# Kernel optimization log

Measured on AMD Instinct MI355X. Metric: run time of the kernel, lower is better.

The kernel has to match this reference:

```python
import jax, jax.numpy as jnp
import numpy as np

B, N, K, D, F, H = 8, 512, 16, 256, 1024, 8


def _ln(x, g, b):
    m = jnp.mean(x, axis=-1, keepdims=True)
    v = jnp.var(x, axis=-1, keepdims=True)
    return (x - m) / jnp.sqrt(v + 1e-5) * g + b


def _mlp(x, W1, b1, W2, b2):
    return jax.nn.gelu(x @ W1 + b1, approximate=False) @ W2 + b2


def setup_inputs() -> dict:
    key = jax.random.key(0)
    ks = jax.random.split(key, 16)
    s = 0.02
    inp = {
        'x': jax.random.normal(ks[0], (N, B, D), jnp.float32),
        'e': jax.random.normal(ks[1], (B, N, K, D), jnp.float32),
        'edge_index': jax.random.randint(ks[2], (B, N, K), 0, N),
        'Wq': jax.random.normal(ks[3], (D, D), jnp.float32) * s,
        'bq': jnp.zeros((D,), jnp.float32),
        'Wk': jax.random.normal(ks[4], (D, D), jnp.float32) * s,
        'bk': jnp.zeros((D,), jnp.float32),
        'Wv': jax.random.normal(ks[5], (D, D), jnp.float32) * s,
        'bv': jnp.zeros((D,), jnp.float32),
        'Wo': jax.random.normal(ks[6], (D, D), jnp.float32) * s,
        'bo': jnp.zeros((D,), jnp.float32),
        'nW1': jax.random.normal(ks[7], (D, F), jnp.float32) * s,
        'nb1': jnp.zeros((F,), jnp.float32),
        'nW2': jax.random.normal(ks[8], (F, D), jnp.float32) * s,
        'nb2': jnp.zeros((D,), jnp.float32),
        'eW1': jax.random.normal(ks[9], (D, F), jnp.float32) * s,
        'eb1': jnp.zeros((F,), jnp.float32),
        'eW2': jax.random.normal(ks[10], (F, D), jnp.float32) * s,
        'eb2': jnp.zeros((D,), jnp.float32),
        'na_g': jnp.ones((D,), jnp.float32), 'na_b': jnp.zeros((D,), jnp.float32),
        'ea_g': jnp.ones((D,), jnp.float32), 'ea_b': jnp.zeros((D,), jnp.float32),
        'nf_g': jnp.ones((D,), jnp.float32), 'nf_b': jnp.zeros((D,), jnp.float32),
        'ef_g': jnp.ones((D,), jnp.float32), 'ef_b': jnp.zeros((D,), jnp.float32),
    }
    return inp


def reference(x, e, edge_index, Wq, bq, Wk, bk, Wv, bv, Wo, bo,
              nW1, nb1, nW2, nb2, eW1, eb1, eW2, eb2,
              na_g, na_b, ea_g, ea_b, nf_g, nf_b, ef_g, ef_b):
    n, b, d = x.shape
    hd = d // H
    xt = jnp.transpose(x, (1, 0, 2))  # (B, N, D) residual in batch-first layout
    bi = jnp.arange(b)[:, None, None]
    ni = jnp.arange(n)[None, :, None]

    # scatter edge features into dense additive attention bias (B, N, N)
    attn_bias = jnp.zeros((b, n, n), x.dtype).at[bi, ni, edge_index].set(e.mean(-1))

    def heads(t):  # (B,N,D) -> (B,H,N,hd)
        return t.reshape(b, n, H, hd).transpose(0, 2, 1, 3)

    q = heads(xt @ Wq + bq) * (hd ** -0.5)
    k = heads(xt @ Wk + bk)
    v = heads(xt @ Wv + bv)
    logits = jnp.einsum('bhnd,bhmd->bhnm', q, k) + attn_bias[:, None]
    attn = jax.nn.softmax(logits, axis=-1)  # (B,H,N,N)
    out = jnp.einsum('bhnm,bhmd->bhnd', attn, v)
    out = out.transpose(0, 2, 1, 3).reshape(b, n, d) @ Wo + bo

    xn = _ln(xt + out, na_g, na_b)  # (B,N,D)

    # edge update: gather attn weights and neighbor node features via edge_index
    weights = attn.mean(axis=1)  # (B,N,N) head-averaged
    w = weights[bi, edge_index, ni]  # (B,N,K): weights[b, edge_index[b,n,k], n]
    gathered = xt[jnp.arange(b)[:, None, None], edge_index]  # (B,N,K,D)
    e2 = _ln(e + w[..., None] * gathered, ea_g, ea_b)

    xn = _ln(xn + _mlp(xn, nW1, nb1, nW2, nb2), nf_g, nf_b)
    e2 = _ln(e2 + _mlp(e2, eW1, eb1, eW2, eb2), ef_g, ef_b)
    return jnp.transpose(xn, (1, 0, 2)), e2
```

## Files before the change

kernel.cpp:

```cpp
#include <hip/hip_runtime.h>
#include <hip/hip_bf16.h>
#include <hip/hip_fp8.h>
#include <math.h>

#define B_ 8
#define N_ 512
#define K_ 16
#define D_ 256
#define F_ 1024
#define H_ 8
#define HD_ 32
#define M_ (B_*N_)
#define R_ (B_*N_*K_)

typedef __bf16 bf16x8 __attribute__((ext_vector_type(8)));
typedef float  f32x4  __attribute__((ext_vector_type(4)));
typedef long   i64x2  __attribute__((ext_vector_type(2)));

__device__ inline short bf16s(float f) {
    __hip_bfloat16 h = __float2bfloat16(f);
    return *reinterpret_cast<short*>(&h);
}
__device__ inline float b2f(short s) {
    union { float f; unsigned u; } v; v.u = ((unsigned)(unsigned short)s) << 16; return v.f;
}
__device__ inline unsigned char f8e4m3(float f) {
    union { __hip_fp8_e4m3 h; unsigned char c; } u;
    u.h = __hip_fp8_e4m3(f);
    return u.c;
}
__device__ __forceinline__ float gelu_f(float x) {
    const float z = fabsf(x) * 0.70710678118654752f;
    const float t = __builtin_amdgcn_rcpf(1.f + 0.3275911f*z);
    const float p = t*(0.254829592f + t*(-0.284496736f + t*(1.421413741f
                  + t*(-1.453152027f + t*1.061405429f))));
    float er = 1.f - p*__expf(-z*z);
    er = (x >= 0.f) ? er : -er;
    return 0.5f*x*(1.f + er);
}
__device__ __forceinline__ int f8pos(int w, int row) {
    return ((((w >> 3) & 3) ^ (row & 3)) << 4) | ((w >> 5) << 3) | (w & 7);
}

__device__ __forceinline__ void gload16(const void* g, void* l) {
    __builtin_amdgcn_global_load_lds(
        (const __attribute__((address_space(1))) unsigned int*)g,
        (__attribute__((address_space(3))) unsigned int*)l, 16, 0, 0);
}

__global__ __launch_bounds__(256) void transposeAll(
        const float* __restrict__ Wq, const float* __restrict__ Wk,
        const float* __restrict__ Wv, const float* __restrict__ Wo,
        const float* __restrict__ nW1, const float* __restrict__ nW2,
        const float* __restrict__ eW1, const float* __restrict__ eW2,
        short* __restrict__ WqkvT, short* __restrict__ WoT,
        short* __restrict__ nW1T, short* __restrict__ nW2T,
        short* __restrict__ eW1T, unsigned char* __restrict__ eW2T8)
{
    const float* W; short* WT = nullptr; int Kk, Nn; float sc = 1.f;
    switch (blockIdx.z) {
        case 0: W=Wq;  WT=WqkvT;          Kk=256;  Nn=256;  sc=0.17677669529663687f; break;
        case 1: W=Wk;  WT=WqkvT+256*256;  Kk=256;  Nn=256;  break;
        case 2: W=Wv;  WT=WqkvT+512*256;  Kk=256;  Nn=256;  break;
        case 3: W=Wo;  WT=WoT;            Kk=256;  Nn=256;  break;
        case 4: W=nW1; WT=nW1T;           Kk=256;  Nn=1024; break;
        case 5: W=nW2; WT=nW2T;           Kk=1024; Nn=256;  break;
        case 6: W=eW1; WT=eW1T;           Kk=256;  Nn=1024; break;
        default:W=eW2;                    Kk=1024; Nn=256;  break;
    }
    const int bx = blockIdx.x, by = blockIdx.y;
    if (bx >= Nn/32 || by >= Kk/32) return;
    __shared__ float tile[32][33];
    int tx = threadIdx.x & 31, ty = threadIdx.x >> 5;
    #pragma unroll
    for (int j = 0; j < 4; ++j) {
        int k = by*32 + ty + j*8;
        tile[ty + j*8][tx] = W[(size_t)k*Nn + bx*32 + tx];
    }
    __syncthreads();
    if (blockIdx.z == 7) {
        #pragma unroll
        for (int j = 0; j < 4; ++j) {
            int n = bx*32 + ty + j*8;
            int k = by*32 + tx;
            int c = k >> 6, w = k & 63;
            eW2T8[(size_t)n*1024 + (c<<6) + f8pos(w, n)] =
                f8e4m3(tile[tx][ty + j*8] * 64.f);
        }
    } else {
        #pragma unroll
        for (int j = 0; j < 4; ++j) {
            int n = bx*32 + ty + j*8;
            WT[(size_t)n*Kk + by*32 + tx] = bf16s(tile[tx][ty + j*8] * sc);
        }
    }
}

__global__ __launch_bounds__(256) void build_bqkv(const float* __restrict__ bq,
        const float* __restrict__ bk, const float* __restrict__ bv,
        float* __restrict__ bqkv)
{
    int t = blockIdx.x*256 + threadIdx.x;
    if (t >= 768) return;
    float v = (t < 256) ? bq[t]*0.17677669529663687f
            : (t < 512) ? bk[t-256] : bv[t-512];
    bqkv[t] = v;
}

__global__ __launch_bounds__(256) void conv_x(const float* __restrict__ x,
        short* __restrict__ xtb)
{
    int row = blockIdx.x;
    int d = threadIdx.x;
    int b = row >> 9, n = row & 511;
    xtb[(size_t)row*D_ + d] = bf16s(x[((size_t)n*B_ + b)*D_ + d]);
}

__global__ __launch_bounds__(256) void edge_means(const float* __restrict__ e,
        float* __restrict__ means)
{
    long row = (long)blockIdx.x*4 + (threadIdx.x >> 6);
    int lane = threadIdx.x & 63;
    float4 v = ((const float4*)(e + row*D_))[lane];
    float s = v.x + v.y + v.z + v.w;
    for (int o = 1; o < 64; o <<= 1) s += __shfl_xor(s, o);
    if (lane == 0) means[row] = s * (1.f/D_);
}

__global__ __launch_bounds__(256) void bias_build(const int* __restrict__ ei,
        const float* __restrict__ means, float* __restrict__ biasb)
{
    const int r0 = blockIdx.x * 16;
    float4* bp4 = (float4*)(biasb + (size_t)r0*N_);
    #pragma unroll
    for (int i = threadIdx.x; i < 16*N_/4; i += 256)
        bp4[i] = make_float4(0.f, 0.f, 0.f, 0.f);
    __syncthreads();
    if (threadIdx.x < 16) {
        const int idx = r0 + threadIdx.x;
        const int* ep = ei + (size_t)idx*K_;
        const float* mp = means + (size_t)idx*K_;
        float* bp = biasb + (size_t)idx*N_;
        for (int k = 0; k < K_; ++k) bp[ep[k]] = mp[k];
    }
}

__global__ __launch_bounds__(256) void gemm_qkv(
        const short* __restrict__ A, const short* __restrict__ BT,
        const float* __restrict__ bias, short* __restrict__ Cb,
        short* __restrict__ vtb, int Kk)
{
    __shared__ __align__(16) short As[128*32];
    __shared__ __align__(16) short Bs[128*32];
    const int t = threadIdx.x;
    const int lane = t & 63;
    const int wave = t >> 6;
    const int wr = (wave >> 1) * 64;
    const int wc = (wave & 1) * 64;
    const int bm = blockIdx.x, bn = blockIdx.y;
    f32x4 acc[4][4] = {};
    const int srow = lane >> 2;
    const int sk   = (lane & 3) * 8;
    const int fr = lane & 15;
    const int fk = (lane >> 4) * 8;
    for (int k0 = 0; k0 < Kk; k0 += 32) {
        __syncthreads();
        #pragma unroll
        for (int i = 0; i < 2; ++i) {
            const int rb = wave*16 + i*64;
            gload16(A  + (size_t)(bm*128 + rb + srow)*Kk + k0 + sk, &As[rb*32]);
            gload16(BT + (size_t)(bn*128 + rb + srow)*Kk + k0 + sk, &Bs[rb*32]);
        }
        __syncthreads();
        bf16x8 af[4], bfr[4];
        #pragma unroll
        for (int i2 = 0; i2 < 4; ++i2)
            af[i2] = *(const bf16x8*)&As[(wr + i2*16 + fr)*32 + fk];
        #pragma unroll
        for (int n2 = 0; n2 < 4; ++n2)
            bfr[n2] = *(const bf16x8*)&Bs[(wc + n2*16 + fr)*32 + fk];
        #pragma unroll
        for (int i2 = 0; i2 < 4; ++i2)
            #pragma unroll
            for (int n2 = 0; n2 < 4; ++n2)
                acc[i2][n2] = __builtin_amdgcn_mfma_f32_16x16x32_bf16(
                        af[i2], bfr[n2], acc[i2][n2], 0, 0, 0);
    }
    const int fq4 = (lane >> 4) * 4;
    #pragma unroll
    for (int i2 = 0; i2 < 4; ++i2) {
        #pragma unroll
        for (int n2 = 0; n2 < 4; ++n2) {
            const int col = bn*128 + wc + n2*16 + fr;
            const float bv = bias[col];
            const int rowb = bm*128 + wr + i2*16 + fq4;
            if (col < 512) {
                #pragma unroll
                for (int r2 = 0; r2 < 4; ++r2)
                    Cb[(size_t)(rowb + r2)*512 + col] = bf16s(acc[i2][n2][r2] + bv);
            } else {
                const int b = rowb >> 9, n = rowb & 511;
                const int dv = col - 512, h = dv >> 5, dh = dv & 31;
                short4 s4;
                s4.x = bf16s(acc[i2][n2][0] + bv);
                s4.y = bf16s(acc[i2][n2][1] + bv);
                s4.z = bf16s(acc[i2][n2][2] + bv);
                s4.w = bf16s(acc[i2][n2][3] + bv);
                *(short4*)&vtb[((size_t)((b*H_ + h)*HD_ + dh))*512 + n] = s4;
            }
        }
    }
}

template<bool F8>
__global__ __launch_bounds__(512, 4) void gemm_gelu(
        const short* __restrict__ A, const short* __restrict__ BT,
        const float* __restrict__ bias, short* __restrict__ Cb,
        unsigned char* __restrict__ C8, int Nn, int Kk)
{
    __shared__ __align__(16) short As[2][128*32];
    __shared__ __align__(16) short Bs[2][256*32];
    const int t = threadIdx.x;
    const int lane = t & 63;
    const int wave = t >> 6;
    const int wrg = (wave >> 2) * 64;
    const int wc  = (wave & 3) * 64;
    const int bm = blockIdx.x, bn = blockIdx.y;
    f32x4 acc[4][4] = {};
    const int srow = lane >> 2;
    const int sk   = (lane & 3) * 8;
    const int fr = lane & 15;
    const int fk = (lane >> 4) * 8;
    auto stage = [&](int s, int k0) {
        {
            const int rb = wave*16;
            gload16(A + (size_t)(bm*128 + rb + srow)*Kk + k0 + sk, &As[s][rb*32]);
        }
        #pragma unroll
        for (int i = 0; i < 2; ++i) {
            const int rb = wave*16 + i*128;
            gload16(BT + (size_t)(bn*256 + rb + srow)*Kk + k0 + sk, &Bs[s][rb*32]);
        }
    };
    stage(0, 0);
    __syncthreads();
    int cur = 0;
    for (int k0 = 0; k0 < Kk; k0 += 32) {
        if (k0 + 32 < Kk) stage(cur ^ 1, k0 + 32);
        bf16x8 af[4], bfr[4];
        #pragma unroll
        for (int i2 = 0; i2 < 4; ++i2)
            af[i2] = *(const bf16x8*)&As[cur][(wrg + i2*16 + fr)*32 + fk];
        #pragma unroll
        for (int n2 = 0; n2 < 4; ++n2)
            bfr[n2] = *(const bf16x8*)&Bs[cur][(wc + n2*16 + fr)*32 + fk];
        #pragma unroll
        for (int i2 = 0; i2 < 4; ++i2)
            #pragma unroll
            for (int n2 = 0; n2 < 4; ++n2)
                acc[i2][n2] = __builtin_amdgcn_mfma_f32_16x16x32_bf16(
                        af[i2], bfr[n2], acc[i2][n2], 0, 0, 0);
        __syncthreads();
        cur ^= 1;
    }
    const int fq4 = (lane >> 4) * 4;
    #pragma unroll
    for (int i2 = 0; i2 < 4; ++i2) {
        #pragma unroll
        for (int n2 = 0; n2 < 4; ++n2) {
            const int col = bn*256 + wc + n2*16 + fr;
            const float bv = bias[col];
            #pragma unroll
            for (int r2 = 0; r2 < 4; ++r2) {
                const int row = bm*128 + wrg + i2*16 + fq4 + r2;
                float v = gelu_f(acc[i2][n2][r2] + bv);
                if constexpr (F8) {
                    const int c = col >> 6, w = col & 63;
                    C8[(size_t)row*1024 + (c<<6) + f8pos(w, row)] = f8e4m3(v * 16.f);
                } else {
                    Cb[(size_t)row*Nn + col] = bf16s(v);
                }
            }
        }
    }
}

template<bool TRANSOUT, int RESMODE, bool DUALOUT>
__global__ __launch_bounds__(512, 4) void gemm_ln2(
        const short* __restrict__ A, const short* __restrict__ BT,
        const float* __restrict__ bias, const float* __restrict__ resf,
        const short* __restrict__ resb,
        const float* __restrict__ g, const float* __restrict__ bt,
        float* __restrict__ out, short* __restrict__ outb, int Kk)
{
    __shared__ __align__(16) short As[2][128*32];
    __shared__ __align__(16) short Bs[2][256*32];
    __shared__ float rs[128][4][2];
    __shared__ float mr[128][2];
    const int t = threadIdx.x;
    const int lane = t & 63;
    const int wave = t >> 6;
    const int wrg = (wave >> 2) * 64;
    const int wc  = (wave & 3) * 64;
    const int bm = blockIdx.x;
    f32x4 acc[4][4] = {};
    const int srow = lane >> 2;
    const int sk   = (lane & 3) * 8;
    const int fr = lane & 15;
    const int fk = (lane >> 4) * 8;
    auto stage = [&](int s, int k0) {
        {
            const int rb = wave*16;
            gload16(A + (size_t)(bm*128 + rb + srow)*Kk + k0 + sk, &As[s][rb*32]);
        }
        #pragma unroll
        for (int i = 0; i < 2; ++i) {
            const int rb = wave*16 + i*128;
            gload16(BT + (size_t)(rb + srow)*Kk + k0 + sk, &Bs[s][rb*32]);
        }
    };
    stage(0, 0);
    __syncthreads();
    int cur = 0;
    for (int k0 = 0; k0 < Kk; k0 += 32) {
        if (k0 + 32 < Kk) stage(cur ^ 1, k0 + 32);
        bf16x8 af[4], bfr[4];
        #pragma unroll
        for (int i2 = 0; i2 < 4; ++i2)
            af[i2] = *(const bf16x8*)&As[cur][(wrg + i2*16 + fr)*32 + fk];
        #pragma unroll
        for (int n2 = 0; n2 < 4; ++n2)
            bfr[n2] = *(const bf16x8*)&Bs[cur][(wc + n2*16 + fr)*32 + fk];
        #pragma unroll
        for (int i2 = 0; i2 < 4; ++i2)
            #pragma unroll
            for (int n2 = 0; n2 < 4; ++n2)
                acc[i2][n2] = __builtin_amdgcn_mfma_f32_16x16x32_bf16(
                        af[i2], bfr[n2], acc[i2][n2], 0, 0, 0);
        __syncthreads();
        cur ^= 1;
    }
    const int fq4 = (lane >> 4) * 4;
    float ps[4][4] = {}, pq[4][4] = {};
    #pragma unroll
    for (int i2 = 0; i2 < 4; ++i2) {
        #pragma unroll
        for (int n2 = 0; n2 < 4; ++n2) {
            const int c = wc + n2*16 + fr;
            const float bv = bias[c];
            #pragma unroll
            for (int r2 = 0; r2 < 4; ++r2) {
                const int row = wrg + i2*16 + fq4 + r2;
                const size_t grow = (size_t)bm*128 + row;
                float rv;
                if constexpr (RESMODE == 1) rv = b2f(resb[grow*256 + c]);
                else if constexpr (RESMODE == 2) {
                    const int bb = (int)(grow >> 9), nn = (int)(grow & 511);
                    rv = resf[((size_t)nn*B_ + bb)*256 + c];
                } else rv = resf[grow*256 + c];
                float v = acc[i2][n2][r2] + bv + rv;
                acc[i2][n2][r2] = v;
                ps[i2][r2] += v;
                pq[i2][r2] += v*v;
            }
        }
    }
    #pragma unroll
    for (int i2 = 0; i2 < 4; ++i2)
        #pragma unroll
        for (int r2 = 0; r2 < 4; ++r2)
            #pragma unroll
            for (int o = 1; o < 16; o <<= 1) {
                ps[i2][r2] += __shfl_xor(ps[i2][r2], o);
                pq[i2][r2] += __shfl_xor(pq[i2][r2], o);
            }
    if ((lane & 15) == 0) {
        #pragma unroll
        for (int i2 = 0; i2 < 4; ++i2)
            #pragma unroll
            for (int r2 = 0; r2 < 4; ++r2) {
                const int row = wrg + i2*16 + fq4 + r2;
                rs[row][wave & 3][0] = ps[i2][r2];
                rs[row][wave & 3][1] = pq[i2][r2];
            }
    }
    __syncthreads();
    if (t < 128) {
        float S = 0.f, Q = 0.f;
        #pragma unroll
        for (int w = 0; w < 4; ++w) { S += rs[t][w][0]; Q += rs[t][w][1]; }
        const float mean = S * (1.f/D_);
        mr[t][0] = mean;
        mr[t][1] = rsqrtf(Q * (1.f/D_) - mean*mean + 1e-5f);
    }
    __syncthreads();
    #pragma unroll
    for (int i2 = 0; i2 < 4; ++i2) {
        #pragma unroll
        for (int n2 = 0; n2 < 4; ++n2) {
            const int c = wc + n2*16 + fr;
            const float gv = g[c], bv2 = bt[c];
            #pragma unroll
            for (int r2 = 0; r2 < 4; ++r2) {
                const int row = wrg + i2*16 + fq4 + r2;
                const size_t grow = (size_t)bm*128 + row;
                const float o = (acc[i2][n2][r2] - mr[row][0])*mr[row][1]*gv + bv2;
                if constexpr (TRANSOUT) {
                    const int bb = (int)(grow >> 9), nn = (int)(grow & 511);
                    out[((size_t)nn*B_ + bb)*D_ + c] = o;
                } else {
                    out[grow*256 + c] = o;
                }
                if constexpr (DUALOUT)
                    outb[grow*256 + c] = bf16s(o);
            }
        }
    }
}

__global__ __launch_bounds__(512, 4) void gemm_ln2f8(
        const unsigned char* __restrict__ A, const unsigned char* __restrict__ BT,
        const float* __restrict__ bias, const short* __restrict__ resb,
        const float* __restrict__ g, const float* __restrict__ bt,
        float* __restrict__ out)
{
    __shared__ __align__(16) unsigned char As[2][128*64];
    __shared__ __align__(16) unsigned char Bs[2][256*64];
    __shared__ float rs[128][4][2];
    __shared__ float mr[128][2];
    const int t = threadIdx.x;
    const int lane = t & 63;
    const int wave = t >> 6;
    const int wrg = (wave >> 2) * 64;
    const int wc  = (wave & 3) * 64;
    const int bm = blockIdx.x;
    f32x4 acc[4][4] = {};
    const int srow = lane >> 2;
    const int skb  = (lane & 3) * 16;
    const int fr = lane & 15;
    const int q16 = (lane >> 4);
    auto stage = [&](int s, int k0) {
        {
            const int rb = wave*16;
            gload16(A + (size_t)(bm*128 + rb + srow)*1024 + k0 + skb, &As[s][rb*64]);
        }
        #pragma unroll
        for (int i = 0; i < 2; ++i) {
            const int rb = wave*16 + i*128;
            gload16(BT + (size_t)(rb + srow)*1024 + k0 + skb, &Bs[s][rb*64]);
        }
    };
    stage(0, 0);
    __syncthreads();
    int cur = 0;
    for (int k0 = 0; k0 < 1024; k0 += 64) {
        if (k0 + 64 < 1024) stage(cur ^ 1, k0 + 64);
        long a8[2][4], b8[2][4];
        #pragma unroll
        for (int i2 = 0; i2 < 4; ++i2) {
            const int ar = wrg + i2*16 + fr;
            const i64x2 av = *(const i64x2*)&As[cur][ar*64 + ((q16 ^ (ar & 3)) << 4)];
            a8[0][i2] = av[0]; a8[1][i2] = av[1];
        }
        #pragma unroll
        for (int n2 = 0; n2 < 4; ++n2) {
            const int br = wc + n2*16 + fr;
            const i64x2 bv = *(const i64x2*)&Bs[cur][br*64 + ((q16 ^ (br & 3)) << 4)];
            b8[0][n2] = bv[0]; b8[1][n2] = bv[1];
        }
        #pragma unroll
        for (int s = 0; s < 2; ++s)
            #pragma unroll
            for (int i2 = 0; i2 < 4; ++i2)
                #pragma unroll
                for (int n2 = 0; n2 < 4; ++n2)
                    acc[i2][n2] = __builtin_amdgcn_mfma_f32_16x16x32_fp8_fp8(
                            a8[s][i2], b8[s][n2], acc[i2][n2], 0, 0, 0);
        __syncthreads();
        cur ^= 1;
    }
    const int fq4 = (lane >> 4) * 4;
    float ps[4][4] = {}, pq[4][4] = {};
    #pragma unroll
    for (int i2 = 0; i2 < 4; ++i2) {
        #pragma unroll
        for (int n2 = 0; n2 < 4; ++n2) {
            const int c = wc + n2*16 + fr;
            const float bv = bias[c];
            #pragma unroll
            for (int r2 = 0; r2 < 4; ++r2) {
                const int row = wrg + i2*16 + fq4 + r2;
                const size_t grow = (size_t)bm*128 + row;
                float v = acc[i2][n2][r2]*(1.f/1024.f) + bv + b2f(resb[grow*256 + c]);
                acc[i2][n2][r2] = v;
                ps[i2][r2] += v;
                pq[i2][r2] += v*v;
            }
        }
    }
    #pragma unroll
    for (int i2 = 0; i2 < 4; ++i2)
        #pragma unroll
        for (int r2 = 0; r2 < 4; ++r2)
            #pragma unroll
            for (int o = 1; o < 16; o <<= 1) {
                ps[i2][r2] += __shfl_xor(ps[i2][r2], o);
                pq[i2][r2] += __shfl_xor(pq[i2][r2], o);
            }
    if ((lane & 15) == 0) {
        #pragma unroll
        for (int i2 = 0; i2 < 4; ++i2)
            #pragma unroll
            for (int r2 = 0; r2 < 4; ++r2) {
                const int row = wrg + i2*16 + fq4 + r2;
                rs[row][wave & 3][0] = ps[i2][r2];
                rs[row][wave & 3][1] = pq[i2][r2];
            }
    }
    __syncthreads();
    if (t < 128) {
        float S = 0.f, Q = 0.f;
        #pragma unroll
        for (int w = 0; w < 4; ++w) { S += rs[t][w][0]; Q += rs[t][w][1]; }
        const float mean = S * (1.f/D_);
        mr[t][0] = mean;
        mr[t][1] = rsqrtf(Q * (1.f/D_) - mean*mean + 1e-5f);
    }
    __syncthreads();
    #pragma unroll
    for (int i2 = 0; i2 < 4; ++i2) {
        #pragma unroll
        for (int n2 = 0; n2 < 4; ++n2) {
            const int c = wc + n2*16 + fr;
            const float gv = g[c], bv2 = bt[c];
            #pragma unroll
            for (int r2 = 0; r2 < 4; ++r2) {
                const int row = wrg + i2*16 + fq4 + r2;
                const size_t grow = (size_t)bm*128 + row;
                out[grow*256 + c] = (acc[i2][n2][r2] - mr[row][0])*mr[row][1]*gv + bv2;
            }
        }
    }
}

__global__ __launch_bounds__(256) void attn_fused(const short* __restrict__ qkb,
        const short* __restrict__ vtb, const float* __restrict__ biasb,
        float* __restrict__ rowsum, short* __restrict__ actx)
{
    __shared__ __align__(16) short Qs[128*32];
    __shared__ __align__(16) short Ks[128*32];
    __shared__ __align__(16) short Vs[32*128];
    __shared__ __align__(16) short Ps[128*128];
    const int it = blockIdx.x, bh = blockIdx.y;
    const int b = bh >> 3, h = bh & 7;
    const int t = threadIdx.x;
    const int lane = t & 63;
    const int wave = t >> 6;
    const int wr0 = wave * 32;
    const int srow = lane >> 2;
    const int sk   = (lane & 3) * 8;
    const int srow8 = lane >> 4;
    const int ck16  = lane & 15;
    const int fr = lane & 15;
    const int fk = (lane >> 4) * 8;
    const int fq4 = (lane >> 4) * 4;
    const int I0 = it * 128;
    #pragma unroll
    for (int i = 0; i < 2; ++i) {
        const int rb = wave*16 + i*64;
        gload16(qkb + (size_t)(b*N_ + I0 + rb + srow)*512 + h*HD_ + sk, &Qs[rb*32]);
    }
    float rsum[2][4] = {};
    f32x4 apv[2][2] = {};
    const float LOG2E = 1.4426950408889634f;
    for (int jt = 0; jt < 4; ++jt) {
        const int J0 = jt * 128;
        __syncthreads();
        #pragma unroll
        for (int i = 0; i < 2; ++i) {
            const int rb = wave*16 + i*64;
            gload16(qkb + (size_t)(b*N_ + J0 + rb + srow)*512 + 256 + h*HD_ + sk, &Ks[rb*32]);
        }
        #pragma unroll
        for (int i = 0; i < 2; ++i) {
            const int db = wave*8 + i*4;
            const int dh = db + srow8;
            gload16(vtb + ((size_t)bh*HD_ + dh)*512 + J0 + ((ck16 ^ (dh & 7)) * 8),
                    &Vs[db*128]);
        }
        __syncthreads();
        bf16x8 aq[2], kf8[8];
        #pragma unroll
        for (int i2 = 0; i2 < 2; ++i2)
            aq[i2] = *(const bf16x8*)&Qs[(wr0 + i2*16 + fr)*32 + fk];
        #pragma unroll
        for (int n2 = 0; n2 < 8; ++n2)
            kf8[n2] = *(const bf16x8*)&Ks[(n2*16 + fr)*32 + fk];
        #pragma unroll
        for (int i2 = 0; i2 < 2; ++i2) {
            #pragma unroll
            for (int n2 = 0; n2 < 8; ++n2) {
                f32x4 z = {0.f, 0.f, 0.f, 0.f};
                f32x4 s = __builtin_amdgcn_mfma_f32_16x16x32_bf16(aq[i2], kf8[n2], z, 0, 0, 0);
                const int jg = J0 + n2*16 + fr;
                #pragma unroll
                for (int r2 = 0; r2 < 4; ++r2) {
                    const int rloc = wr0 + i2*16 + fq4 + r2;
                    const float l = s[r2] + biasb[((size_t)b*N_ + I0 + rloc)*N_ + jg];
                    const float p = exp2f(fminf(l, 80.f) * LOG2E);
                    rsum[i2][r2] += p;
                    int idx = rloc*128 + n2*16 + fr;
                    idx ^= (rloc & 7) << 3;
                    Ps[idx] = bf16s(p);
                }
            }
        }
        __syncthreads();
        #pragma unroll
        for (int ks = 0; ks < 4; ++ks) {
            bf16x8 ap[2], bv[2];
            #pragma unroll
            for (int i2 = 0; i2 < 2; ++i2) {
                const int r = wr0 + i2*16 + fr;
                int idx = r*128 + ks*32 + fk;
                idx ^= (r & 7) << 3;
                ap[i2] = *(const bf16x8*)&Ps[idx];
            }
            #pragma unroll
            for (int n2 = 0; n2 < 2; ++n2) {
                const int dh = n2*16 + fr;
                const int q = lane >> 4;
                const int slot = (ks*4 + q) ^ (dh & 7);
                bv[n2] = *(const bf16x8*)&Vs[dh*128 + slot*8];
            }
            #pragma unroll
            for (int i2 = 0; i2 < 2; ++i2)
                #pragma unroll
                for (int n2 = 0; n2 < 2; ++n2)
                    apv[i2][n2] = __builtin_amdgcn_mfma_f32_16x16x32_bf16(
                            ap[i2], bv[n2], apv[i2][n2], 0, 0, 0);
        }
    }
    #pragma unroll
    for (int i2 = 0; i2 < 2; ++i2)
        #pragma unroll
        for (int r2 = 0; r2 < 4; ++r2)
            #pragma unroll
            for (int o = 1; o < 16; o <<= 1)
                rsum[i2][r2] += __shfl_xor(rsum[i2][r2], o);
    #pragma unroll
    for (int i2 = 0; i2 < 2; ++i2) {
        #pragma unroll
        for (int r2 = 0; r2 < 4; ++r2) {
            const int row = wr0 + i2*16 + fq4 + r2;
            if (fr == 0)
                rowsum[(size_t)bh*N_ + I0 + row] = rsum[i2][r2];
            const float inv = 1.f / rsum[i2][r2];
            #pragma unroll
            for (int n2 = 0; n2 < 2; ++n2)
                actx[((size_t)b*N_ + I0 + row)*D_ + h*HD_ + n2*16 + fr]
                    = bf16s(apv[i2][n2][r2] * inv);
        }
    }
}

__device__ inline void ln_core(float v[4], int lane, const float* __restrict__ g,
        const float* __restrict__ bt, float out[4])
{
    float s  = v[0] + v[1] + v[2] + v[3];
    float sq = v[0]*v[0] + v[1]*v[1] + v[2]*v[2] + v[3]*v[3];
    for (int o = 1; o < 64; o <<= 1) { s += __shfl_xor(s, o); sq += __shfl_xor(sq, o); }
    float mean = s * (1.f/D_);
    float rstd = rsqrtf(sq * (1.f/D_) - mean*mean + 1e-5f);
    const float4 gv = *(const float4*)(g  + lane*4);
    const float4 bv = *(const float4*)(bt + lane*4);
    out[0] = (v[0]-mean)*rstd*gv.x + bv.x;
    out[1] = (v[1]-mean)*rstd*gv.y + bv.y;
    out[2] = (v[2]-mean)*rstd*gv.z + bv.z;
    out[3] = (v[3]-mean)*rstd*gv.w + bv.w;
}

__global__ __launch_bounds__(256) void edge_update(const float* __restrict__ e,
        const float* __restrict__ x, const int* __restrict__ ei,
        const short* __restrict__ qkb, const float* __restrict__ biasb,
        const float* __restrict__ rowsum, const float* __restrict__ g,
        const float* __restrict__ bt, short* __restrict__ e2b)
{
    long row = (long)blockIdx.x*4 + (threadIdx.x >> 6);
    int lane = threadIdx.x & 63;
    long bi = row >> 4;
    long b = bi / N_; int i = (int)(bi % N_);
    int ej = ei[row];
    const short4 q4 = *(const short4*)(qkb + ((size_t)b*N_ + ej)*512 + lane*4);
    const short4 k4 = *(const short4*)(qkb + ((size_t)b*N_ + i)*512 + 256 + lane*4);
    float dot = b2f(q4.x)*b2f(k4.x) + b2f(q4.y)*b2f(k4.y)
              + b2f(q4.z)*b2f(k4.z) + b2f(q4.w)*b2f(k4.w);
    dot += __shfl_xor(dot, 1); dot += __shfl_xor(dot, 2); dot += __shfl_xor(dot, 4);
    const int h = lane >> 3;
    const float l = dot + biasb[((size_t)b*N_ + ej)*N_ + i];
    float p = exp2f(fminf(l, 80.f) * 1.4426950408889634f)
            / rowsum[((size_t)b*H_ + h)*N_ + ej];
    p += __shfl_xor(p, 8); p += __shfl_xor(p, 16); p += __shfl_xor(p, 32);
    const float w = p * (1.f/H_);
    const float4 ev = *(const float4*)(e + row*D_ + lane*4);
    const float4 xv = *(const float4*)(x + ((size_t)ej*B_ + b)*D_ + lane*4);
    float v[4] = {ev.x + w*xv.x, ev.y + w*xv.y, ev.z + w*xv.z, ev.w + w*xv.w};
    float o[4];
    ln_core(v, lane, g, bt, o);
    short4 s4; s4.x = bf16s(o[0]); s4.y = bf16s(o[1]); s4.z = bf16s(o[2]); s4.w = bf16s(o[3]);
    *(short4*)(e2b + row*D_ + lane*4) = s4;
}

extern "C" void kernel_launch(void* const* d_in, const int* in_sizes, int n_in,
                              void* d_out, int out_size, void* d_ws, size_t ws_size,
                              hipStream_t stream)
{
    (void)in_sizes; (void)n_in; (void)out_size; (void)ws_size;
    const float* x    = (const float*)d_in[0];
    const float* e    = (const float*)d_in[1];
    const int*   ei   = (const int*)d_in[2];
    const float* Wq   = (const float*)d_in[3];
    const float* bq   = (const float*)d_in[4];
    const float* Wk   = (const float*)d_in[5];
    const float* bk   = (const float*)d_in[6];
    const float* Wv   = (const float*)d_in[7];
    const float* bv   = (const float*)d_in[8];
    const float* Wo   = (const float*)d_in[9];
    const float* bo   = (const float*)d_in[10];
    const float* nW1  = (const float*)d_in[11];
    const float* nb1  = (const float*)d_in[12];
    const float* nW2  = (const float*)d_in[13];
    const float* nb2  = (const float*)d_in[14];
    const float* eW1  = (const float*)d_in[15];
    const float* eb1  = (const float*)d_in[16];
    const float* eW2  = (const float*)d_in[17];
    const float* eb2  = (const float*)d_in[18];
    const float* na_g = (const float*)d_in[19];
    const float* na_b = (const float*)d_in[20];
    const float* ea_g = (const float*)d_in[21];
    const float* ea_b = (const float*)d_in[22];
    const float* nf_g = (const float*)d_in[23];
    const float* nf_b = (const float*)d_in[24];
    const float* ef_g = (const float*)d_in[25];
    const float* ef_b = (const float*)d_in[26];

    float* out1 = (float*)d_out;
    float* e2f  = out1 + (size_t)N_*B_*D_;

    char* wp = (char*)d_ws;
    auto alloc = [&](size_t bytes) -> char* {
        char* p = wp; wp += (bytes + 255) & ~(size_t)255; return p;
    };
    short* WqkvT  = (short*)alloc((size_t)768*D_*2);
    float* bqkv   = (float*)alloc(768*4);
    short* WoT    = (short*)alloc((size_t)D_*D_*2);
    short* nW1T   = (short*)alloc((size_t)F_*D_*2);
    short* nW2T   = (short*)alloc((size_t)D_*F_*2);
    short* eW1T   = (short*)alloc((size_t)F_*D_*2);
    unsigned char* eW2T8 = (unsigned char*)alloc((size_t)D_*F_);
    float* rowsum = (float*)alloc((size_t)B_*H_*N_*4);
    short* e2b    = (short*)alloc((size_t)R_*D_*2);
    char* ov = wp;
    auto allocA = [&](size_t bytes) -> char* {
        char* p = ov; ov += (bytes + 255) & ~(size_t)255; return p;
    };
    short* xtb    = (short*)allocA((size_t)M_*D_*2);
    float* means  = (float*)allocA((size_t)R_*4);
    float* biasb  = (float*)allocA((size_t)B_*N_*N_*4);
    short* qkb    = (short*)allocA((size_t)M_*512*2);
    short* vtb    = (short*)allocA((size_t)B_*H_*HD_*N_*2);
    short* actx   = (short*)allocA((size_t)M_*D_*2);
    float* xn     = (float*)allocA((size_t)M_*D_*4);
    short* xnb    = (short*)allocA((size_t)M_*D_*2);
    short* nhid   = (short*)allocA((size_t)M_*F_*2);
    unsigned char* ehid8 = (unsigned char*)wp;

    transposeAll<<<dim3(32, 32, 8), 256, 0, stream>>>(Wq, Wk, Wv, Wo,
            nW1, nW2, eW1, eW2, WqkvT, WoT, nW1T, nW2T, eW1T, eW2T8);
    build_bqkv<<<3, 256, 0, stream>>>(bq, bk, bv, bqkv);
    conv_x<<<M_, 256, 0, stream>>>(x, xtb);

    edge_means<<<R_/4, 256, 0, stream>>>(e, means);
    bias_build<<<M_/16, 256, 0, stream>>>(ei, means, biasb);

    gemm_qkv<<<dim3(M_/128, 768/128), 256, 0, stream>>>(
            xtb, WqkvT, bqkv, qkb, vtb, D_);

    attn_fused<<<dim3(N_/128, B_*H_), 256, 0, stream>>>(qkb, vtb, biasb, rowsum, actx);

    gemm_ln2<false,2,true><<<M_/128, 512, 0, stream>>>(
            actx, WoT, bo, x, nullptr, na_g, na_b, xn, xnb, D_);

    gemm_gelu<false><<<dim3(M_/128, F_/256), 512, 0, stream>>>(
            xnb, nW1T, nb1, nhid, nullptr, F_, D_);
    gemm_ln2<true,0,false><<<M_/128, 512, 0, stream>>>(
            nhid, nW2T, nb2, xn, nullptr, nf_g, nf_b, out1, nullptr, F_);

    edge_update<<<R_/4, 256, 0, stream>>>(e, x, ei, qkb, biasb, rowsum,
            ea_g, ea_b, e2b);
    gemm_gelu<true><<<dim3(R_/128, F_/256), 512, 0, stream>>>(
            e2b, eW1T, eb1, nullptr, ehid8, F_, D_);
    gemm_ln2f8<<<R_/128, 512, 0, stream>>>(
            ehid8, eW2T8, eb2, e2b, ef_g, ef_b, e2f);
}
```

Before: 319.1 us.

## Permute hidden dimension so GELU epilogue writes packed 4-element vectors

Applies a permutation (hperm) to the F-dimension of the intermediate activation. nW2T and eW2T8 are re-laid out to match, so each lane's four n2 columns become contiguous. The GEMM+GELU epilogue can then store four bf16 values as one short4, or four fp8 values as one packed 32-bit word via cvt_pk_fp8, instead of scattered scalar stores. This cuts store instruction count and uncoalesced byte writes. In exchange, correctness now depends on the permutation being applied consistently in the weight transpose and the downstream GEMM.

```diff
diff --git a/kernel.cpp b/kernel.cpp
--- a/kernel.cpp
+++ b/kernel.cpp
@@ -40,6 +40,9 @@
 }
 __device__ __forceinline__ int f8pos(int w, int row) {
     return ((((w >> 3) & 3) ^ (row & 3)) << 4) | ((w >> 5) << 3) | (w & 7);
+}
+__device__ __forceinline__ int hperm(int k) {
+    return (k & ~63) | ((k & 15) << 2) | ((k >> 4) & 3);
 }
 
 __device__ __forceinline__ void gload16(const void* g, void* l) {
@@ -82,10 +85,15 @@
         #pragma unroll
         for (int j = 0; j < 4; ++j) {
             int n = bx*32 + ty + j*8;
-            int k = by*32 + tx;
-            int c = k >> 6, w = k & 63;
-            eW2T8[(size_t)n*1024 + (c<<6) + f8pos(w, n)] =
+            int kp = hperm(by*32 + tx);
+            eW2T8[(size_t)n*1024 + (kp & ~63) + f8pos(kp & 63, n)] =
                 f8e4m3(tile[tx][ty + j*8] * 64.f);
+        }
+    } else if (blockIdx.z == 5) {
+        #pragma unroll
+        for (int j = 0; j < 4; ++j) {
+            int n = bx*32 + ty + j*8;
+            WT[(size_t)n*1024 + hperm(by*32 + tx)] = bf16s(tile[tx][ty + j*8]);
         }
     } else {
         #pragma unroll
@@ -264,22 +272,26 @@
         cur ^= 1;
     }
     const int fq4 = (lane >> 4) * 4;
+    const int chunk = (bn*4 + (wc >> 6)) * 64;
     #pragma unroll
     for (int i2 = 0; i2 < 4; ++i2) {
         #pragma unroll
-        for (int n2 = 0; n2 < 4; ++n2) {
-            const int col = bn*256 + wc + n2*16 + fr;
-            const float bv = bias[col];
-            #pragma unroll
-            for (int r2 = 0; r2 < 4; ++r2) {
-                const int row = bm*128 + wrg + i2*16 + fq4 + r2;
-                float v = gelu_f(acc[i2][n2][r2] + bv);
-                if constexpr (F8) {
-                    const int c = col >> 6, w = col & 63;
-                    C8[(size_t)row*1024 + (c<<6) + f8pos(w, row)] = f8e4m3(v * 16.f);
-                } else {
-                    Cb[(size_t)row*Nn + col] = bf16s(v);
-                }
+        for (int r2 = 0; r2 < 4; ++r2) {
+            const int row = bm*128 + wrg + i2*16 + fq4 + r2;
+            float v[4];
+            #pragma unroll
+            for (int n2 = 0; n2 < 4; ++n2)
+                v[n2] = gelu_f(acc[i2][n2][r2] + bias[bn*256 + wc + n2*16 + fr]);
+            if constexpr (F8) {
+                int word = __builtin_amdgcn_cvt_pk_fp8_f32(v[0]*16.f, v[1]*16.f, 0, false);
+                word = __builtin_amdgcn_cvt_pk_fp8_f32(v[2]*16.f, v[3]*16.f, word, true);
+                *(unsigned int*)(C8 + (size_t)row*1024 + chunk + f8pos(fr*4, row))
+                    = (unsigned int)word;
+            } else {
+                short4 s4;
+                s4.x = bf16s(v[0]); s4.y = bf16s(v[1]);
+                s4.z = bf16s(v[2]); s4.w = bf16s(v[3]);
+                *(short4*)&Cb[(size_t)row*1024 + chunk + fr*4] = s4;
             }
         }
     }
```

Result: no change. 315.4 us (-1.2%).
